# Performance work log

Hardware: AMD Instinct MI355X
Metric: run time of the kernel (lower is better)

## Reference

```python
import jax, jax.numpy as jnp
import numpy as np

M, K, N, GROUP = 4096, 4096, 14336, 64


def setup_inputs() -> dict:
    key = jax.random.key(0)
    k1, k2, k3 = jax.random.split(key, 3)
    x = jax.random.normal(k1, (M, K), dtype=jnp.float32)
    # int4 quantized weight values in [0, 15], symmetric around zero-point 8
    q_weight = jax.random.randint(k2, (K, N), 0, 16, dtype=jnp.int32)
    # per-group scales: one scale per GROUP rows of k, per output column
    scales = jax.random.uniform(k3, (K // GROUP, N), dtype=jnp.float32) * 0.02
    return {"x": x, "q_weight": q_weight, "scales": scales, "group_size": GROUP}


def reference(x, q_weight, scales, group_size):
    # Marlin int4 GEMM math (act_order=False): dequantize per k-group, then GEMM.
    k, n = q_weight.shape
    g = k // group_size
    # (q - 8) * scale, scale broadcast over each group of `group_size` k-rows
    w = (q_weight.reshape(g, group_size, n).astype(scales.dtype) - 8.0) * scales[:, None, :]
    w = w.reshape(k, n)  # [K, N] dequantized weight
    return x @ w  # [M, N]
```

## Files before the change

kernel.cpp:

```cpp
#include <hip/hip_runtime.h>

#define MDIM 4096
#define KDIM 4096
#define NDIM 14336

typedef __attribute__((ext_vector_type(8))) short bf16x8;
typedef __attribute__((ext_vector_type(4))) short bf16x4;
typedef __attribute__((ext_vector_type(4))) float f32x4;

__device__ __forceinline__ unsigned short f2bf(float f) {
  unsigned u = __float_as_uint(f);
  return (unsigned short)((u + 0x7FFFu + ((u >> 16) & 1u)) >> 16);
}

__device__ __forceinline__ void async_copy16(const void* g, void* l) {
  __builtin_amdgcn_global_load_lds((const __attribute__((address_space(1))) unsigned*)g,
                                   (__attribute__((address_space(3))) unsigned*)l, 16, 0, 0);
}

__device__ __forceinline__ bf16x8 ds_read_b128(const short* p) {
  bf16x8 r;
  auto lp = (const __attribute__((address_space(3))) short*)p;
  asm volatile("ds_read_b128 %0, %1" : "=v"(r) : "v"(lp));
  return r;
}

__global__ __launch_bounds__(256) void cvt_x_kernel(const float* __restrict__ X,
                                                    short* __restrict__ Xb) {
  const int i = blockIdx.x * 256 + threadIdx.x;
  const float4* p = (const float4*)X + (size_t)i * 2;
  const float4 a = p[0], b = p[1];
  bf16x8 v;
  v[0] = f2bf(a.x); v[1] = f2bf(a.y); v[2] = f2bf(a.z); v[3] = f2bf(a.w);
  v[4] = f2bf(b.x); v[5] = f2bf(b.y); v[6] = f2bf(b.z); v[7] = f2bf(b.w);
  *((bf16x8*)Xb + i) = v;
}

constexpr int DQ_STRIDE = 264;
__global__ __launch_bounds__(512) void dequant_w_kernel(const int* __restrict__ Q,
                                                        const float* __restrict__ S,
                                                        short* __restrict__ Wt) {
  __shared__ short Ls[128 * DQ_STRIDE];
  const int k0 = blockIdx.x * 256;
  const int n0 = blockIdx.y * 128;
  const int t  = threadIdx.x;

  const int n4  = (t & 31) * 4;
  const int rbi = (t >> 5) * 4;
#pragma unroll
  for (int kc = 0; kc < 4; ++kc) {
    const int g  = (k0 >> 6) + kc;
    const int kb = k0 + kc * 64 + rbi;
    const float4 s4 = *(const float4*)(S + (size_t)g * NDIM + n0 + n4);
    int4 q[4];
#pragma unroll
    for (int i = 0; i < 4; ++i)
      q[i] = *(const int4*)(Q + (size_t)(kb + i) * NDIM + n0 + n4);
    short* lp = &Ls[n4 * DQ_STRIDE + kc * 64 + rbi];
    bf16x4 v;
    v[0] = (short)f2bf((float)(q[0].x - 8) * s4.x);
    v[1] = (short)f2bf((float)(q[1].x - 8) * s4.x);
    v[2] = (short)f2bf((float)(q[2].x - 8) * s4.x);
    v[3] = (short)f2bf((float)(q[3].x - 8) * s4.x);
    *(bf16x4*)(lp + 0 * DQ_STRIDE) = v;
    v[0] = (short)f2bf((float)(q[0].y - 8) * s4.y);
    v[1] = (short)f2bf((float)(q[1].y - 8) * s4.y);
    v[2] = (short)f2bf((float)(q[2].y - 8) * s4.y);
    v[3] = (short)f2bf((float)(q[3].y - 8) * s4.y);
    *(bf16x4*)(lp + 1 * DQ_STRIDE) = v;
    v[0] = (short)f2bf((float)(q[0].z - 8) * s4.z);
    v[1] = (short)f2bf((float)(q[1].z - 8) * s4.z);
    v[2] = (short)f2bf((float)(q[2].z - 8) * s4.z);
    v[3] = (short)f2bf((float)(q[3].z - 8) * s4.z);
    *(bf16x4*)(lp + 2 * DQ_STRIDE) = v;
    v[0] = (short)f2bf((float)(q[0].w - 8) * s4.w);
    v[1] = (short)f2bf((float)(q[1].w - 8) * s4.w);
    v[2] = (short)f2bf((float)(q[2].w - 8) * s4.w);
    v[3] = (short)f2bf((float)(q[3].w - 8) * s4.w);
    *(bf16x4*)(lp + 3 * DQ_STRIDE) = v;
  }
  __syncthreads();

  const int c = (t & 7) * 8;
#pragma unroll
  for (int p = 0; p < 2; ++p) {
    const int nr = (t >> 3) + p * 64;
    const short* lr = &Ls[nr * DQ_STRIDE + c];
    short* wp = Wt + (size_t)(n0 + nr) * KDIM + k0 + c;
#pragma unroll
    for (int r = 0; r < 4; ++r)
      *(bf16x8*)(wp + r * 64) = *(const bf16x8*)(lr + r * 64);
  }
}

__global__ __launch_bounds__(512, 1)
void gemm_bf16tt(const short* __restrict__ Xb, const short* __restrict__ Wt,
                 float* __restrict__ Out) {
  __shared__ short As[2][256 * 64];
  __shared__ short Bs[2][256 * 64];

  const int bm = blockIdx.x * 256;
  const int bn = blockIdx.y * 256;
  const int tid = threadIdx.x, lane = tid & 63, wave = tid >> 6;
  const int wr = wave >> 2;
  const int wc = wave & 3;
  const int quad = lane >> 4, l16 = lane & 15;
  const int lx = l16 & 7;

  f32x4 acc[8][4];
#pragma unroll
  for (int i = 0; i < 8; ++i)
#pragma unroll
    for (int j = 0; j < 4; ++j) acc[i][j] = (f32x4){0.f, 0.f, 0.f, 0.f};

  const int row0 = tid >> 3;
  const int kof  = ((tid & 7) ^ (row0 & 7)) * 8;
  const size_t aoff = (size_t)(bm + row0) * KDIM + kof;
  const size_t boff = (size_t)(bn + row0) * KDIM + kof;
  const int ldst_off = wave * 8 * 64;

#define STAGE_G(buf, g, kt1)                                                          \
  do {                                                                                \
    const short* gsrc = (((g) < 2) ? (Xb + aoff) : (Wt + boff)) +                     \
                        (size_t)((g) & 1) * 128 * KDIM + (size_t)(kt1) * 64;          \
    short* ldst = (((g) < 2) ? As[buf] : Bs[buf]) + (((g) & 1) * 128) * 64 + ldst_off;\
    async_copy16(gsrc, ldst);                                                         \
    async_copy16(gsrc + (size_t)64 * KDIM, ldst + 64 * 64);                           \
  } while (0)

#define PHASE_COMPUTE(cur, mh, nh)                                                    \
  do {                                                                                \
    const short* Ab = As[cur];                                                        \
    const short* Bb = Bs[cur];                                                        \
    bf16x8 af[4][2], bv[2][2];                                                        \
    _Pragma("unroll") for (int s = 0; s < 2; ++s) {                                   \
      const int sl = (((s * 4 + quad)) ^ lx) << 3;                                    \
      _Pragma("unroll") for (int i = 0; i < 4; ++i)                                   \
        af[i][s] = ds_read_b128(&Ab[(wr * 128 + ((mh) * 4 + i) * 16 + l16) * 64 + sl]);\
      _Pragma("unroll") for (int j = 0; j < 2; ++j)                                   \
        bv[j][s] = ds_read_b128(&Bb[(wc * 64 + ((nh) * 2 + j) * 16 + l16) * 64 + sl]);\
    }                                                                                 \
    asm volatile("s_waitcnt lgkmcnt(0)" ::: "memory");                                \
    __builtin_amdgcn_sched_barrier(0);                                                \
    __builtin_amdgcn_s_setprio(1);                                                    \
    _Pragma("unroll") for (int i = 0; i < 4; ++i)                                     \
      _Pragma("unroll") for (int j = 0; j < 2; ++j)                                   \
        _Pragma("unroll") for (int s = 0; s < 2; ++s)                                 \
          acc[(mh) * 4 + i][(nh) * 2 + j] = __builtin_amdgcn_mfma_f32_16x16x32_bf16(  \
              af[i][s], bv[j][s], acc[(mh) * 4 + i][(nh) * 2 + j], 0, 0, 0);          \
    __builtin_amdgcn_s_setprio(0);                                                    \
  } while (0)

  constexpr int NT = KDIM / 64;

#pragma unroll
  for (int g = 0; g < 4; ++g) STAGE_G(0, g, 0);

  for (int kt = 0; kt < NT; ++kt) {
    const int cur = kt & 1, nxt = cur ^ 1;
    const bool pre = (kt + 1 < NT);
    __builtin_amdgcn_s_barrier();
    __builtin_amdgcn_sched_barrier(0);
    if (pre) {
      STAGE_G(nxt, 0, kt + 1);
      asm volatile("s_waitcnt vmcnt(2)" ::: "memory");
    } else {
      asm volatile("s_waitcnt vmcnt(0)" ::: "memory");
    }
    __builtin_amdgcn_s_barrier();
    __builtin_amdgcn_sched_barrier(0);
    PHASE_COMPUTE(cur, 0, 0);
    if (pre) STAGE_G(nxt, 1, kt + 1);
    PHASE_COMPUTE(cur, 0, 1);
    if (pre) STAGE_G(nxt, 2, kt + 1);
    PHASE_COMPUTE(cur, 1, 0);
    if (pre) STAGE_G(nxt, 3, kt + 1);
    PHASE_COMPUTE(cur, 1, 1);
  }
#undef STAGE_G
#undef PHASE_COMPUTE

#pragma unroll
  for (int i = 0; i < 8; ++i) {
    const int r0 = bm + wr * 128 + i * 16 + quad * 4;
#pragma unroll
    for (int j = 0; j < 4; ++j) {
      const int col = bn + wc * 64 + j * 16 + l16;
#pragma unroll
      for (int r = 0; r < 4; ++r)
        Out[(size_t)(r0 + r) * NDIM + col] = acc[i][j][r];
    }
  }
}

constexpr int BKP = 72;
__global__ __launch_bounds__(256, 2)
void marlin_int4_gemm(const float* __restrict__ X, const int* __restrict__ Q,
                      const float* __restrict__ S, float* __restrict__ Out) {
  __shared__ short As[128 * BKP];
  __shared__ short Bs[128 * BKP];
  const int bm = blockIdx.x * 128, bn = blockIdx.y * 128;
  const int tid = threadIdx.x, lane = tid & 63, wave = tid >> 6;
  const int wm = (wave & 1) * 64, wn = (wave >> 1) * 64;
  const int quad = lane >> 4, l16 = lane & 15;
  const int nB = tid & 127, krB = (tid >> 7) * 32;
  f32x4 acc[4][4];
#pragma unroll
  for (int i = 0; i < 4; ++i)
#pragma unroll
    for (int j = 0; j < 4; ++j) acc[i][j] = (f32x4){0.f, 0.f, 0.f, 0.f};
  for (int kt = 0; kt < KDIM / 64; ++kt) {
    const int k0 = kt * 64;
    const float s = S[kt * NDIM + bn + nB];
    const float bias = -8.0f * s;
    __syncthreads();
#pragma unroll
    for (int i = 0; i < 8; ++i) {
      const int idx4 = tid + (i << 8);
      const int row = idx4 >> 4, col = (idx4 & 15) << 2;
      const float4 v = *(const float4*)(X + (size_t)(bm + row) * KDIM + k0 + col);
      ushort4 b;
      b.x = f2bf(v.x); b.y = f2bf(v.y); b.z = f2bf(v.z); b.w = f2bf(v.w);
      *(ushort4*)(&As[row * BKP + col]) = b;
    }
    unsigned short wb[32];
#pragma unroll
    for (int j = 0; j < 32; ++j) {
      const int qv = Q[(size_t)(k0 + krB + j) * NDIM + bn + nB];
      wb[j] = f2bf((float)qv * s + bias);
    }
    {
      short* brow = &Bs[nB * BKP + krB];
#pragma unroll
      for (int c = 0; c < 4; ++c) {
        bf16x8 v;
#pragma unroll
        for (int e = 0; e < 8; ++e) v[e] = (short)wb[c * 8 + e];
        *(bf16x8*)(brow + c * 8) = v;
      }
    }
    __syncthreads();
#pragma unroll
    for (int kk = 0; kk < 64; kk += 32) {
      bf16x8 af[4], bfr[4];
#pragma unroll
      for (int i = 0; i < 4; ++i)
        af[i] = *(const bf16x8*)&As[(wm + i * 16 + l16) * BKP + kk + quad * 8];
#pragma unroll
      for (int j = 0; j < 4; ++j)
        bfr[j] = *(const bf16x8*)&Bs[(wn + j * 16 + l16) * BKP + kk + quad * 8];
#pragma unroll
      for (int i = 0; i < 4; ++i)
#pragma unroll
        for (int j = 0; j < 4; ++j)
          acc[i][j] = __builtin_amdgcn_mfma_f32_16x16x32_bf16(af[i], bfr[j], acc[i][j], 0, 0, 0);
    }
  }
#pragma unroll
  for (int i = 0; i < 4; ++i) {
    const int r0 = bm + wm + i * 16 + quad * 4;
#pragma unroll
    for (int j = 0; j < 4; ++j) {
      const int col = bn + wn + j * 16 + l16;
#pragma unroll
      for (int r = 0; r < 4; ++r)
        Out[(size_t)(r0 + r) * NDIM + col] = acc[i][j][r];
    }
  }
}

extern "C" void kernel_launch(void* const* d_in, const int* in_sizes, int n_in,
                              void* d_out, int out_size, void* d_ws, size_t ws_size,
                              hipStream_t stream) {
  const float* X = (const float*)d_in[0];
  const int*   Q = (const int*)d_in[1];
  const float* S = (const float*)d_in[2];
  float* Out = (float*)d_out;

  const size_t xb_elems = (size_t)MDIM * KDIM;
  const size_t wt_elems = (size_t)NDIM * KDIM;
  const size_t need = (xb_elems + wt_elems) * sizeof(short);

  if (ws_size >= need) {
    short* Xb = (short*)d_ws;
    short* Wt = Xb + xb_elems;
    cvt_x_kernel<<<(int)(xb_elems / 8 / 256), 256, 0, stream>>>(X, Xb);
    dequant_w_kernel<<<dim3(KDIM / 256, NDIM / 128), 512, 0, stream>>>(Q, S, Wt);
    gemm_bf16tt<<<dim3(MDIM / 256, NDIM / 256), 512, 0, stream>>>(Xb, Wt, Out);
  } else {
    marlin_int4_gemm<<<dim3(MDIM / 128, NDIM / 128), 256, 0, stream>>>(X, Q, S, Out);
  }
}
```

Measured before the change: 880.5 us.

## Restructure bf16 GEMM k-loop into barrier-separated read/MFMA phases

The main loop of the bf16 GEMM now splits the 64-wide k tile into two 32-wide halves. Each half loads all eight A fragments once and reuses them across both N halves, and extra workgroup barriers separate the LDS-read and MFMA phases, interleaved with the async global-to-LDS prefetch stages. The goal is fewer redundant A fragment reads and tighter read/compute alternation across waves. The launch bound also changes to request two blocks per CU. That squeezes the register budget for a kernel holding a 128-float accumulator and may force spills, while the 128 KB of LDS per block may still not allow a second resident block.

Result: slower. 912.3 us (+3.6%).

```diff
diff --git a/kernel.cpp b/kernel.cpp
--- a/kernel.cpp
+++ b/kernel.cpp
@@ -93,7 +93,7 @@
   }
 }
 
-__global__ __launch_bounds__(512, 1)
+__global__ __launch_bounds__(512, 2)
 void gemm_bf16tt(const short* __restrict__ Xb, const short* __restrict__ Wt,
                  float* __restrict__ Out) {
   __shared__ short As[2][256 * 64];
@@ -128,28 +128,27 @@
     async_copy16(gsrc + (size_t)64 * KDIM, ldst + 64 * 64);                           \
   } while (0)
 
-#define PHASE_COMPUTE(cur, mh, nh)                                                    \
+#define DSREAD_A(s)                                                                   \
+  _Pragma("unroll") for (int i = 0; i < 8; ++i)                                       \
+      af[i] = ds_read_b128(&Ab[(wr * 128 + i * 16 + l16) * 64 + (((s)*4 + quad) ^ lx) * 8]);
+#define DSREAD_B(s, nh)                                                               \
+  _Pragma("unroll") for (int j = 0; j < 2; ++j)                                       \
+      bv[j] = ds_read_b128(&Bb[(wc * 64 + ((nh)*2 + j) * 16 + l16) * 64 + (((s)*4 + quad) ^ lx) * 8]);
+#define MFMA16(nh)                                                                    \
   do {                                                                                \
-    const short* Ab = As[cur];                                                        \
-    const short* Bb = Bs[cur];                                                        \
-    bf16x8 af[4][2], bv[2][2];                                                        \
-    _Pragma("unroll") for (int s = 0; s < 2; ++s) {                                   \
-      const int sl = (((s * 4 + quad)) ^ lx) << 3;                                    \
-      _Pragma("unroll") for (int i = 0; i < 4; ++i)                                   \
-        af[i][s] = ds_read_b128(&Ab[(wr * 128 + ((mh) * 4 + i) * 16 + l16) * 64 + sl]);\
+    __builtin_amdgcn_s_setprio(1);                                                    \
+    _Pragma("unroll") for (int i = 0; i < 8; ++i)                                     \
       _Pragma("unroll") for (int j = 0; j < 2; ++j)                                   \
-        bv[j][s] = ds_read_b128(&Bb[(wc * 64 + ((nh) * 2 + j) * 16 + l16) * 64 + sl]);\
-    }                                                                                 \
-    asm volatile("s_waitcnt lgkmcnt(0)" ::: "memory");                                \
-    __builtin_amdgcn_sched_barrier(0);                                                \
-    __builtin_amdgcn_s_setprio(1);                                                    \
-    _Pragma("unroll") for (int i = 0; i < 4; ++i)                                     \
-      _Pragma("unroll") for (int j = 0; j < 2; ++j)                                   \
-        _Pragma("unroll") for (int s = 0; s < 2; ++s)                                 \
-          acc[(mh) * 4 + i][(nh) * 2 + j] = __builtin_amdgcn_mfma_f32_16x16x32_bf16(  \
-              af[i][s], bv[j][s], acc[(mh) * 4 + i][(nh) * 2 + j], 0, 0, 0);          \
+        acc[i][(nh)*2 + j] = __builtin_amdgcn_mfma_f32_16x16x32_bf16(                 \
+            af[i], bv[j], acc[i][(nh)*2 + j], 0, 0, 0);                               \
     __builtin_amdgcn_s_setprio(0);                                                    \
   } while (0)
+#define WAIT_LGK()                                                                    \
+  asm volatile("s_waitcnt lgkmcnt(0)" ::: "memory");                                  \
+  __builtin_amdgcn_sched_barrier(0)
+#define BAR()                                                                         \
+  __builtin_amdgcn_s_barrier();                                                       \
+  __builtin_amdgcn_sched_barrier(0)
 
   constexpr int NT = KDIM / 64;
 
@@ -159,26 +158,48 @@
   for (int kt = 0; kt < NT; ++kt) {
     const int cur = kt & 1, nxt = cur ^ 1;
     const bool pre = (kt + 1 < NT);
-    __builtin_amdgcn_s_barrier();
-    __builtin_amdgcn_sched_barrier(0);
+    const short* Ab = As[cur];
+    const short* Bb = Bs[cur];
+    bf16x8 af[8], bv[2];
+
     if (pre) {
       STAGE_G(nxt, 0, kt + 1);
       asm volatile("s_waitcnt vmcnt(2)" ::: "memory");
     } else {
       asm volatile("s_waitcnt vmcnt(0)" ::: "memory");
     }
-    __builtin_amdgcn_s_barrier();
-    __builtin_amdgcn_sched_barrier(0);
-    PHASE_COMPUTE(cur, 0, 0);
+    BAR();
+    DSREAD_A(0);
+    DSREAD_B(0, 0);
+    WAIT_LGK();
+    MFMA16(0);
+    BAR();
+    DSREAD_B(0, 1);
     if (pre) STAGE_G(nxt, 1, kt + 1);
-    PHASE_COMPUTE(cur, 0, 1);
+    BAR();
+    WAIT_LGK();
+    MFMA16(1);
+    BAR();
+    DSREAD_A(1);
+    DSREAD_B(1, 0);
     if (pre) STAGE_G(nxt, 2, kt + 1);
-    PHASE_COMPUTE(cur, 1, 0);
+    BAR();
+    WAIT_LGK();
+    MFMA16(0);
+    BAR();
+    DSREAD_B(1, 1);
     if (pre) STAGE_G(nxt, 3, kt + 1);
-    PHASE_COMPUTE(cur, 1, 1);
+    BAR();
+    WAIT_LGK();
+    MFMA16(1);
+    BAR();
   }
 #undef STAGE_G
-#undef PHASE_COMPUTE
+#undef DSREAD_A
+#undef DSREAD_B
+#undef MFMA16
+#undef WAIT_LGK
+#undef BAR
 
 #pragma unroll
   for (int i = 0; i < 8; ++i) {
```
